# Optimization experiments

Measured on AMD Instinct MI355X. Metric: run time of the kernel, lower is better.

The kernel has to match this reference:

```python
import jax, jax.numpy as jnp
import numpy as np

H, KVH, HD, E, TOPK = 16, 4, 128, 8, 2
EPS = 1.1920929e-07  # fp32 machine eps, matches F.rms_norm default


def _rms(v):
    return v * jax.lax.rsqrt(jnp.mean(jnp.square(v), axis=-1, keepdims=True) + EPS)


def _rope(t, cos, sin):
    d = t.shape[-1] // 2
    t1, t2 = t[..., :d], t[..., d:]
    return jnp.concatenate([t1 * cos + t2 * sin, -t1 * sin + t2 * cos], axis=-1)


def setup_inputs():
    key = jax.random.key(0)
    ks = jax.random.split(key, 10)
    B, T, C, D = 2, 1024, 2048, 512
    # real rotary tables (broadcast over batch and heads)
    inv = 1.0 / (10000.0 ** (np.arange(HD // 2, dtype=np.float64) / (HD // 2)))
    ang = np.arange(T, dtype=np.float64)[:, None] * inv[None, :]
    cos = jnp.asarray(np.cos(ang), jnp.float32)[None, :, None, :]
    sin = jnp.asarray(np.sin(ang), jnp.float32)[None, :, None, :]
    w = lambda k, shp, fan: jax.random.normal(k, shp, jnp.float32) * (fan ** -0.5)
    return {
        'x': jax.random.normal(ks[0], (B, T, C), jnp.float32),
        'cos': cos, 'sin': sin,
        'Wq': w(ks[1], (C, C), C),
        'Wk': w(ks[2], (C, KVH * HD), C),
        'Wv': w(ks[3], (C, KVH * HD), C),
        'Wo': w(ks[4], (C, C), C),
        'Wr': w(ks[5], (C, E), C),
        'Ws1': w(ks[6], (C, D), C),
        'Ws2': w(ks[7], (D, C), D),
        'We1': w(ks[8], (E, C, D), C),
        'We2': w(ks[9], (E, D, C), D),
    }


def reference(x, cos, sin, Wq, Wk, Wv, Wo, Wr, Ws1, Ws2, We1, We2):
    B, T, C = x.shape
    # ---- attention (pre-norm, RoPE, QK-norm, GQA, causal SDPA) ----
    xn = _rms(x)
    q = _rms(_rope((xn @ Wq).reshape(B, T, H, HD), cos, sin))      # [B,T,H,HD]
    k = _rms(_rope((xn @ Wk).reshape(B, T, KVH, HD), cos, sin))    # [B,T,KVH,HD]
    v = (xn @ Wv).reshape(B, T, KVH, HD)
    rep = H // KVH
    k = jnp.repeat(k, rep, axis=2)
    v = jnp.repeat(v, rep, axis=2)
    scores = jnp.einsum('bthd,bshd->bhts', q, k) / np.float32(np.sqrt(HD))
    causal = jnp.tril(jnp.ones((T, T), bool))
    scores = jnp.where(causal, scores, jnp.float32(-np.inf))
    att = jax.nn.softmax(scores, axis=-1)
    y = jnp.einsum('bhts,bshd->bthd', att, v).reshape(B, T, C) @ Wo
    x = x + y
    # ---- DeepSeekMoE (shared expert + top-k routed experts) ----
    xf = _rms(x).reshape(-1, C)                                    # [N,C]
    N = xf.shape[0]
    shared = jnp.square(jax.nn.relu(xf @ Ws1)) @ Ws2               # [N,C]
    logits = xf @ Wr                                               # [N,E]
    tk_w, tk_idx = jax.lax.top_k(logits, TOPK)
    tk_w = jax.nn.softmax(tk_w.astype(jnp.float32), axis=-1).astype(x.dtype)
    # scatter top-k probs into dense per-expert gates (indices unique per row)
    gates = jnp.zeros((N, E), x.dtype).at[jnp.arange(N)[:, None], tk_idx].set(tk_w)
    h = jnp.square(jax.nn.relu(jnp.einsum('nc,ecd->end', xf, We1)))  # [E,N,D]
    routed = jnp.einsum('end,edc,ne->nc', h, We2, gates)             # [N,C]
    return x + (shared + routed).reshape(B, T, C)
```

## Files before the change

### kernel.cpp

```cpp
#include <hip/hip_runtime.h>

typedef _Float16 h16;
typedef _Float16 half8 __attribute__((ext_vector_type(8)));
typedef float f32x4 __attribute__((ext_vector_type(4)));

#define EPS_RMS 1.1920929e-07f
#define MiB (1ull << 20)

__device__ __forceinline__ void gload_lds16(const void* g, void* l) {
  __builtin_amdgcn_global_load_lds(
      (const __attribute__((address_space(1))) unsigned int*)g,
      (__attribute__((address_space(3))) unsigned int*)l, 16, 0, 0);
}

struct GemmP {
  const h16* Ah; const h16* Al;
  const h16* Bh; const h16* Bl;
  float* Cf; h16* Ch; h16* Cl;
  const float* R;
  const int* cnt; const int* off; const int* perm;
  long sAz, sBz, sCzHi, sCzLo;
  int M, N, K, lda, ldb, ldc;
  int zAoff, zBoff, zCoff, bzShift, czHiShift, czLoMask;
  float outScale;
};

template <int SPLIT, int EPI, int USECNT, int GATHER, int ASYNC>
__global__ __launch_bounds__(256, 4) void gemm_k(GemmP p) {
  constexpr int NP = SPLIT ? 2 : 1;
  constexpr int NBUF = (ASYNC == 1) ? 2 : 1;
  constexpr int APAD = (ASYNC == 1) ? 32 : 40;
  constexpr int BPAD = (ASYNC >= 1) ? 32 : 40;
  __shared__ __align__(16) h16 As[NBUF][NP][128][APAD];
  __shared__ __align__(16) h16 Bs[NBUF][NP][128][BPAD];
  __shared__ int permLds[GATHER ? 128 : 1];

  int bm, bn, zl;
  if constexpr (USECNT) {
    const int flat2d = blockIdx.y * gridDim.x + blockIdx.x;
    zl = flat2d & 7;
    const int idx = (flat2d >> 3) * 8 + blockIdx.z;
    bm = idx % gridDim.x;
    bn = idx / gridDim.x;
  } else {
    const int nwg = gridDim.x * gridDim.y;
    const int flat = blockIdx.y * gridDim.x + blockIdx.x;
    const int q8 = nwg >> 3, r8 = nwg & 7;
    const int xcd = flat & 7, sub = flat >> 3;
    const int swz = (xcd < r8 ? xcd * (q8 + 1) : r8 * (q8 + 1) + (xcd - r8) * q8) + sub;
    bm = swz % gridDim.x;
    bn = swz / gridDim.x;
    zl = blockIdx.z;
  }

  int Meff, rowbase;
  if (USECNT) {
    Meff = p.cnt[zl]; rowbase = p.off[zl];
    if (bm * 128 >= Meff) return;
  } else { Meff = p.M; rowbase = 0; }

  const int zA = zl + p.zAoff, zB = zl + p.zBoff, zC = zl + p.zCoff;
  const h16* Ah = p.Ah + (size_t)zA * p.sAz;
  const h16* Al = SPLIT ? p.Al + (size_t)zA * p.sAz : (const h16*)0;
  const size_t bofs = (size_t)(zB >> p.bzShift) * p.sBz;
  const h16* Bh = p.Bh + bofs;
  const h16* Bl = SPLIT ? p.Bl + bofs : (const h16*)0;
  const size_t cofs = (size_t)(zC >> p.czHiShift) * p.sCzHi +
                      (size_t)(zC & p.czLoMask) * p.sCzLo;

  const int tid = threadIdx.x;
  const int lane = tid & 63;
  const int wid = tid >> 6, wr = wid >> 1, wc = wid & 1;
  const int fr = lane & 15, fq = lane >> 4;

  if (GATHER) {
    if (tid < 128) {
      const int local = bm * 128 + tid;
      permLds[tid] = (local < Meff) ? p.perm[rowbase + local] : -1;
    }
    __syncthreads();
  }

  const long arow0 = (long)rowbase + (long)bm * 128;

  const f32x4 fz = {0.f, 0.f, 0.f, 0.f};
  f32x4 acc[4][4];
#pragma unroll
  for (int m = 0; m < 4; ++m)
#pragma unroll
    for (int n = 0; n < 4; ++n) acc[m][n] = fz;

  const int nkt = p.K / 32;

  auto compute = [&](int buf) {
    half8 af[NP][4], bf[NP][4];
#pragma unroll
    for (int m = 0; m < 4; ++m) {
      const int r = wr * 64 + m * 16 + fr;
      af[0][m] = *(const half8*)&As[buf][0][r][fq * 8];
      if (SPLIT) af[1][m] = *(const half8*)&As[buf][1][r][fq * 8];
    }
#pragma unroll
    for (int n = 0; n < 4; ++n) {
      const int c = wc * 64 + n * 16 + fr;
      bf[0][n] = *(const half8*)&Bs[buf][0][c][fq * 8];
      if (SPLIT) bf[1][n] = *(const half8*)&Bs[buf][1][c][fq * 8];
    }
#pragma unroll
    for (int m = 0; m < 4; ++m)
#pragma unroll
      for (int n = 0; n < 4; ++n) {
        acc[m][n] = __builtin_amdgcn_mfma_f32_16x16x32_f16(af[0][m], bf[0][n], acc[m][n], 0, 0, 0);
        if (SPLIT) {
          acc[m][n] = __builtin_amdgcn_mfma_f32_16x16x32_f16(af[0][m], bf[1][n], acc[m][n], 0, 0, 0);
          acc[m][n] = __builtin_amdgcn_mfma_f32_16x16x32_f16(af[1][m], bf[0][n], acc[m][n], 0, 0, 0);
        }
      }
  };

  if constexpr (ASYNC == 1) {
    auto stage = [&](int buf, int kt) {
      const int kb = kt * 32;
#pragma unroll
      for (int it = 0; it < 2; ++it) {
        const int d = (tid + it * 256) * 16;
        const int row = d >> 6;
        const int oct = (d >> 4) & 3;
        const size_t gb = ((size_t)(bn * 128 + row)) * p.ldb + kb + oct * 8;
        gload_lds16(Bh + gb, (char*)&Bs[buf][0][0][0] + d);
        if (SPLIT) gload_lds16(Bl + gb, (char*)&Bs[buf][1][0][0] + d);
        const size_t ga = (size_t)(arow0 + row) * p.lda + kb + oct * 8;
        gload_lds16(Ah + ga, (char*)&As[buf][0][0][0] + d);
        if (SPLIT) gload_lds16(Al + ga, (char*)&As[buf][1][0][0] + d);
      }
    };
    stage(0, 0);
    __syncthreads();
    int cur = 0;
    for (int kt = 0; kt < nkt; ++kt) {
      if (kt + 1 < nkt) stage(cur ^ 1, kt + 1);
      compute(cur);
      __syncthreads();
      cur ^= 1;
    }
  } else {
    for (int kt = 0; kt < nkt; ++kt) {
      if (kt) __syncthreads();
      const int kb = kt * 32;
      if constexpr (ASYNC == 2) {
#pragma unroll
        for (int it = 0; it < 2; ++it) {
          const int d = (tid + it * 256) * 16;
          const int row = d >> 6;
          const int oct = (d >> 4) & 3;
          const size_t gb = ((size_t)(bn * 128 + row)) * p.ldb + kb + oct * 8;
          gload_lds16(Bh + gb, (char*)&Bs[0][0][0][0] + d);
          if (SPLIT) gload_lds16(Bl + gb, (char*)&Bs[0][1][0][0] + d);
        }
      }
#pragma unroll
      for (int s = 0; s < 2; ++s) {
        const int seg = tid * 2 + s;
        const int row = seg >> 2, ks = (seg & 3) * 8;
        const int local = bm * 128 + row;
        bool av; long arow;
        if (GATHER) { const int tk2 = permLds[row]; av = (tk2 >= 0); arow = tk2; }
        else { av = (local < Meff); arow = (long)rowbase + local; }
        half8 vh = {0,0,0,0,0,0,0,0}, vl = {0,0,0,0,0,0,0,0};
        if (av) {
          vh = *(const half8*)(Ah + arow * (size_t)p.lda + kb + ks);
          if (SPLIT) vl = *(const half8*)(Al + arow * (size_t)p.lda + kb + ks);
        }
        *(half8*)&As[0][0][row][ks] = vh;
        if (SPLIT) *(half8*)&As[0][1][row][ks] = vl;
        if constexpr (ASYNC == 0) {
          const long brow = (long)bn * 128 + row;
          *(half8*)&Bs[0][0][row][ks] = *(const half8*)(Bh + brow * (size_t)p.ldb + kb + ks);
          if (SPLIT)
            *(half8*)&Bs[0][1][row][ks] = *(const half8*)(Bl + brow * (size_t)p.ldb + kb + ks);
        }
      }
      __syncthreads();
      compute(0);
    }
  }

#pragma unroll
  for (int m = 0; m < 4; ++m)
#pragma unroll
    for (int n = 0; n < 4; ++n)
#pragma unroll
      for (int j = 0; j < 4; ++j) {
        const int rl = wr * 64 + m * 16 + fq * 4 + j;
        const int cl = wc * 64 + n * 16 + fr;
        const int local = bm * 128 + rl;
        if (local >= Meff) continue;
        const size_t idx = cofs + ((size_t)rowbase + local) * p.ldc + (size_t)bn * 128 + cl;
        const float v = acc[m][n][j] * p.outScale;
        if (EPI == 0) p.Cf[idx] = v;
        else if (EPI == 1) p.Cf[idx] = v + p.R[idx];
        else if (EPI == 2) {
          const h16 hh = (h16)v;
          p.Ch[idx] = hh; p.Cl[idx] = (h16)(v - (float)hh);
        } else if (EPI == 3) {
          const float r2 = v > 0.f ? v * v : 0.f;
          p.Ch[idx] = (h16)r2;
        } else {
          p.Ch[idx] = (h16)v;
        }
      }
}

__global__ __launch_bounds__(512, 1) void flash_k(
    const h16* __restrict__ Qh, const h16* __restrict__ Ql,
    const h16* __restrict__ Kh, const h16* __restrict__ Kl,
    const h16* __restrict__ Vh, const h16* __restrict__ Vl,
    h16* __restrict__ yh, h16* __restrict__ yl) {
  __shared__ __align__(16) h16 Ks[2][32][136];
  __shared__ __align__(16) h16 Vs[2][128][40];
  __shared__ __align__(16) h16 Ps[8][2][16][40];

  const int qb = blockIdx.x, z = blockIdx.y;
  const int b = z >> 4, h = z & 15;
  const size_t qoff = (size_t)z * 131072;
  const size_t koff = (size_t)(b * 4 + (h >> 2)) * 131072;

  const int tid = threadIdx.x;
  const int lane = tid & 63, w = tid >> 6;
  const int fr = lane & 15, fq = lane >> 4;

  const int qrow = qb * 128 + w * 16 + fr;
  half8 qa[2][4];
#pragma unroll
  for (int kt = 0; kt < 4; ++kt) {
    qa[0][kt] = *(const half8*)(Qh + qoff + (size_t)qrow * 128 + kt * 32 + fq * 8);
    qa[1][kt] = *(const half8*)(Ql + qoff + (size_t)qrow * 128 + kt * 32 + fq * 8);
  }

  const int kRow = tid >> 4, kSeg = tid & 15;
  const int vRow = tid >> 2, vSeg = tid & 3;

  const f32x4 fz = {0.f, 0.f, 0.f, 0.f};
  f32x4 y[8];
#pragma unroll
  for (int n = 0; n < 8; ++n) y[n] = fz;
  float mrow[4] = {-3.0e38f, -3.0e38f, -3.0e38f, -3.0e38f};
  float lrow[4] = {0.f, 0.f, 0.f, 0.f};

  const int nt = (qb + 1) * 4;
  for (int t = 0; t < nt; ++t) {
    const int kvb = t * 32;
    if (t) __syncthreads();
#pragma unroll
    for (int pl = 0; pl < 2; ++pl) {
      const h16* kp = pl ? Kl : Kh;
      const h16* vp = pl ? Vl : Vh;
      *(half8*)&Ks[pl][kRow][kSeg * 8] =
          *(const half8*)(kp + koff + (size_t)(kvb + kRow) * 128 + kSeg * 8);
      *(half8*)&Vs[pl][vRow][vSeg * 8] =
          *(const half8*)(vp + koff + (size_t)vRow * 1024 + kvb + vSeg * 8);
    }
    __syncthreads();

    f32x4 sf[2] = {fz, fz};
#pragma unroll
    for (int n = 0; n < 2; ++n)
#pragma unroll
      for (int kt = 0; kt < 4; ++kt) {
        const half8 bh2 = *(const half8*)&Ks[0][n * 16 + fr][kt * 32 + fq * 8];
        const half8 bl2 = *(const half8*)&Ks[1][n * 16 + fr][kt * 32 + fq * 8];
        sf[n] = __builtin_amdgcn_mfma_f32_16x16x32_f16(qa[0][kt], bh2, sf[n], 0, 0, 0);
        sf[n] = __builtin_amdgcn_mfma_f32_16x16x32_f16(qa[0][kt], bl2, sf[n], 0, 0, 0);
        sf[n] = __builtin_amdgcn_mfma_f32_16x16x32_f16(qa[1][kt], bh2, sf[n], 0, 0, 0);
      }

    if (kvb + 31 > qb * 128) {
#pragma unroll
      for (int n = 0; n < 2; ++n)
#pragma unroll
        for (int j = 0; j < 4; ++j) {
          const int kvg = kvb + n * 16 + fr;
          const int qg = qb * 128 + w * 16 + fq * 4 + j;
          if (kvg > qg) sf[n][j] = -3.0e38f;
        }
    }

    float al[4];
#pragma unroll
    for (int j = 0; j < 4; ++j) {
      float tm = fmaxf(sf[0][j], sf[1][j]);
#pragma unroll
      for (int msk = 1; msk < 16; msk <<= 1) tm = fmaxf(tm, __shfl_xor(tm, msk, 16));
      const float mn = fmaxf(mrow[j], tm);
      al[j] = __expf(mrow[j] - mn);
      mrow[j] = mn;
      sf[0][j] = __expf(sf[0][j] - mn);
      sf[1][j] = __expf(sf[1][j] - mn);
      float ts = sf[0][j] + sf[1][j];
#pragma unroll
      for (int msk = 1; msk < 16; msk <<= 1) ts += __shfl_xor(ts, msk, 16);
      lrow[j] = lrow[j] * al[j] + ts;
    }
#pragma unroll
    for (int n = 0; n < 8; ++n)
#pragma unroll
      for (int j = 0; j < 4; ++j) y[n][j] *= al[j];

#pragma unroll
    for (int n = 0; n < 2; ++n)
#pragma unroll
      for (int j = 0; j < 4; ++j) {
        const float pp = sf[n][j] * 1024.f;
        const h16 hh = (h16)pp;
        Ps[w][0][fq * 4 + j][n * 16 + fr] = hh;
        Ps[w][1][fq * 4 + j][n * 16 + fr] = (h16)(pp - (float)hh);
      }

    const half8 pah = *(const half8*)&Ps[w][0][fr][fq * 8];
    const half8 pal = *(const half8*)&Ps[w][1][fr][fq * 8];
#pragma unroll
    for (int n = 0; n < 8; ++n) {
      const half8 vh2 = *(const half8*)&Vs[0][n * 16 + fr][fq * 8];
      const half8 vl2 = *(const half8*)&Vs[1][n * 16 + fr][fq * 8];
      y[n] = __builtin_amdgcn_mfma_f32_16x16x32_f16(pah, vh2, y[n], 0, 0, 0);
      y[n] = __builtin_amdgcn_mfma_f32_16x16x32_f16(pah, vl2, y[n], 0, 0, 0);
      y[n] = __builtin_amdgcn_mfma_f32_16x16x32_f16(pal, vh2, y[n], 0, 0, 0);
    }
  }

#pragma unroll
  for (int n = 0; n < 8; ++n)
#pragma unroll
    for (int j = 0; j < 4; ++j) {
      const int row = qb * 128 + w * 16 + fq * 4 + j;
      const int col = h * 128 + n * 16 + fr;
      const float v = y[n][j] / (1024.f * lrow[j]);
      const size_t idx = ((size_t)(b * 1024 + row)) * 2048 + col;
      const h16 hh = (h16)v;
      yh[idx] = hh; yl[idx] = (h16)(v - (float)hh);
    }
}

__global__ void tsplit_k(const float* __restrict__ W, h16* __restrict__ Th,
                         h16* __restrict__ Tl, int K, int N, float scale, int wantLo) {
  const size_t eoff = (size_t)blockIdx.z * (size_t)K * N;
  W += eoff; Th += eoff; if (Tl) Tl += eoff;
  __shared__ float tile[32][33];
  const int nt = blockIdx.x * 32, kt = blockIdx.y * 32;
  const int c = threadIdx.x & 31, r0 = threadIdx.x >> 5;
#pragma unroll
  for (int rr = 0; rr < 4; ++rr)
    tile[r0 + rr * 8][c] = W[(size_t)(kt + r0 + rr * 8) * N + nt + c];
  __syncthreads();
#pragma unroll
  for (int rr = 0; rr < 4; ++rr) {
    const int nrow = nt + r0 + rr * 8;
    const float v = tile[c][r0 + rr * 8] * scale;
    const h16 hh = (h16)v;
    Th[(size_t)nrow * K + kt + c] = hh;
    if (wantLo) Tl[(size_t)nrow * K + kt + c] = (h16)(v - (float)hh);
  }
}

template <int WLO, int WSC>
__global__ void rms_k(const float* __restrict__ X, h16* __restrict__ H,
                      h16* __restrict__ L, float* __restrict__ SC) {
  const int row = blockIdx.x;
  const float* x = X + (size_t)row * 2048;
  __shared__ float red[256];
  const int tid = threadIdx.x;
  float ss = 0.f;
  for (int c = tid; c < 2048; c += 256) { const float v = x[c]; ss += v * v; }
  red[tid] = ss; __syncthreads();
  for (int t = 128; t > 0; t >>= 1) {
    if (tid < t) red[tid] += red[tid + t];
    __syncthreads();
  }
  const float sc = rsqrtf(red[0] * (1.f / 2048.f) + EPS_RMS);
  if (WSC && tid == 0) SC[row] = sc;
  for (int c = tid; c < 2048; c += 256) {
    const float v = x[c] * sc;
    const size_t o2 = (size_t)row * 2048 + c;
    const h16 hh = (h16)v;
    H[o2] = hh;
    if (WLO) L[o2] = (h16)(v - (float)hh);
  }
}

__global__ void rope_k(const float* __restrict__ qkv, const float* __restrict__ cosT,
                       const float* __restrict__ sinT,
                       h16* __restrict__ Qh, h16* __restrict__ Ql,
                       h16* __restrict__ Kh, h16* __restrict__ Kl,
                       h16* __restrict__ Vh, h16* __restrict__ Vl) {
  const int tok = blockIdx.x;
  const int b = tok >> 10, t = tok & 1023;
  const int u = blockIdx.y, d = threadIdx.x;
  __shared__ float buf[128];
  __shared__ float red[128];
  int col;
  if (u < 16) col = u * 128 + d;
  else if (u < 20) col = 2048 + (u - 16) * 128 + d;
  else col = 2560 + (u - 20) * 128 + d;
  float v = qkv[(size_t)tok * 3072 + col];
  if (u < 20) {
    buf[d] = v; __syncthreads();
    float r;
    if (d < 64) {
      const float c = cosT[t * 64 + d], s = sinT[t * 64 + d];
      r = buf[d] * c + buf[d + 64] * s;
    } else {
      const float c = cosT[t * 64 + d - 64], s = sinT[t * 64 + d - 64];
      r = -buf[d - 64] * s + buf[d] * c;
    }
    red[d] = r * r; __syncthreads();
    for (int tt = 64; tt > 0; tt >>= 1) {
      if (d < tt) red[d] += red[d + tt];
      __syncthreads();
    }
    v = r * rsqrtf(red[0] * (1.f / 128.f) + EPS_RMS);
    if (u < 16) v *= 0.08838834764831845f;
  }
  const h16 hh = (h16)v;
  const h16 lo = (h16)(v - (float)hh);
  if (u < 16) {
    const size_t o2 = (((size_t)(b * 16 + u)) * 1024 + t) * 128 + d;
    Qh[o2] = hh; Ql[o2] = lo;
  } else if (u < 20) {
    const size_t o2 = (((size_t)(b * 4 + (u - 16))) * 1024 + t) * 128 + d;
    Kh[o2] = hh; Kl[o2] = lo;
  } else {
    const size_t o2 = ((size_t)(b * 4 + (u - 20))) * 131072 + (size_t)d * 1024 + t;
    Vh[o2] = hh; Vl[o2] = lo;
  }
}

__global__ void router_k(const float* __restrict__ x2, const float* __restrict__ rowscale,
                         const float* __restrict__ Wr,
                         int* __restrict__ idx2, float* __restrict__ g2,
                         int* __restrict__ cnt) {
  const int n = blockIdx.x;
  const int tid = threadIdx.x;
  __shared__ float red[256][8];
  float part[8] = {0, 0, 0, 0, 0, 0, 0, 0};
  for (int c = tid; c < 2048; c += 256) {
    const float v = x2[(size_t)n * 2048 + c];
    const float* w2 = Wr + (size_t)c * 8;
#pragma unroll
    for (int e = 0; e < 8; ++e) part[e] += v * w2[e];
  }
#pragma unroll
  for (int e = 0; e < 8; ++e) red[tid][e] = part[e];
  __syncthreads();
  for (int t = 128; t > 0; t >>= 1) {
    if (tid < t)
#pragma unroll
      for (int e = 0; e < 8; ++e) red[tid][e] += red[tid + t][e];
    __syncthreads();
  }
  if (tid == 0) {
    const float sc = rowscale[n];
    float l[8];
#pragma unroll
    for (int e = 0; e < 8; ++e) l[e] = red[0][e] * sc;
    int i1 = 0;
    for (int e = 1; e < 8; ++e) if (l[e] > l[i1]) i1 = e;
    int i2 = (i1 == 0) ? 1 : 0;
    for (int e = 0; e < 8; ++e) if (e != i1 && l[e] > l[i2]) i2 = e;
    const float e2 = __expf(l[i2] - l[i1]);
    const float inv = 1.f / (1.f + e2);
    idx2[n * 2] = i1; idx2[n * 2 + 1] = i2;
    g2[n * 2] = inv; g2[n * 2 + 1] = e2 * inv;
    atomicAdd(&cnt[i1], 1); atomicAdd(&cnt[i2], 1);
  }
}

__global__ void zero8_k(int* __restrict__ p) {
  if (threadIdx.x < 8 && blockIdx.x == 0) p[threadIdx.x] = 0;
}

__global__ void scan_k(const int* __restrict__ cnt, int* __restrict__ off,
                       int* __restrict__ base) {
  if (threadIdx.x == 0 && blockIdx.x == 0) {
    int a = 0;
    for (int e = 0; e < 8; ++e) { off[e] = a; base[e] = a; a += cnt[e]; }
  }
}

__global__ void assign_k(const int* __restrict__ idx2, int* __restrict__ base,
                         int* __restrict__ perm, int* __restrict__ pos2) {
  const int n = blockIdx.x * 256 + threadIdx.x;
  if (n >= 2048) return;
  for (int j = 0; j < 2; ++j) {
    const int e = idx2[n * 2 + j];
    const int pos = atomicAdd(&base[e], 1);
    perm[pos] = n;
    pos2[n * 2 + j] = pos;
  }
}

__global__ void combine_k(const float* __restrict__ x2, const h16* __restrict__ sh,
                          const h16* __restrict__ rp, const int* __restrict__ pos2,
                          const float* __restrict__ g2, float* __restrict__ out) {
  const int n = blockIdx.x;
  const int p0 = pos2[n * 2], p1 = pos2[n * 2 + 1];
  const float g0 = g2[n * 2], g1 = g2[n * 2 + 1];
  for (int c = threadIdx.x; c < 2048; c += 256) {
    const size_t i = (size_t)n * 2048 + c;
    out[i] = x2[i] + (float)sh[i] + g0 * (float)rp[(size_t)p0 * 2048 + c]
             + g1 * (float)rp[(size_t)p1 * 2048 + c];
  }
}

extern "C" void kernel_launch(void* const* d_in, const int* in_sizes, int n_in,
                              void* d_out, int out_size, void* d_ws, size_t ws_size,
                              hipStream_t stream) {
  const float* x    = (const float*)d_in[0];
  const float* cosT = (const float*)d_in[1];
  const float* sinT = (const float*)d_in[2];
  const float* Wq   = (const float*)d_in[3];
  const float* Wk   = (const float*)d_in[4];
  const float* Wv   = (const float*)d_in[5];
  const float* Wo   = (const float*)d_in[6];
  const float* Wr   = (const float*)d_in[7];
  const float* Ws1  = (const float*)d_in[8];
  const float* Ws2  = (const float*)d_in[9];
  const float* We1  = (const float*)d_in[10];
  const float* We2  = (const float*)d_in[11];
  float* out = (float*)d_out;

  unsigned char* W = (unsigned char*)d_ws;
  int*   idx2     = (int*)(W + 0);
  float* g2       = (float*)(W + 16 * 1024);
  int*   cnt      = (int*)(W + 32 * 1024);
  int*   offs     = (int*)(W + 33 * 1024);
  int*   base     = (int*)(W + 34 * 1024);
  int*   perm     = (int*)(W + 36 * 1024);
  int*   pos2     = (int*)(W + 52 * 1024);
  float* rowscale = (float*)(W + 68 * 1024);
  h16* W1h = (h16*)(W + 1 * MiB);
  h16* W1l = (h16*)(W + 13 * MiB);
  h16* W2h = (h16*)(W + 1 * MiB);
  h16* W2l = (h16*)(W + 9 * MiB);
  h16* xnh = (h16*)(W + 25 * MiB);
  h16* xnl = (h16*)(W + 33 * MiB);
  h16* yh  = (h16*)(W + 25 * MiB);
  h16* yl  = (h16*)(W + 33 * MiB);
  h16* xfh = (h16*)(W + 25 * MiB);
  h16* shh = (h16*)(W + 33 * MiB);
  float* qkv = (float*)(W + 41 * MiB);
  h16* hs    = (h16*)(W + 41 * MiB);
  h16* hperm = (h16*)(W + 43 * MiB);
  h16* Qh = (h16*)(W + 65 * MiB);
  h16* Ql = (h16*)(W + 73 * MiB);
  h16* Kh = (h16*)(W + 81 * MiB);
  h16* Kl = (h16*)(W + 83 * MiB);
  h16* Vh = (h16*)(W + 85 * MiB);
  h16* Vl = (h16*)(W + 87 * MiB);
  h16* rph = (h16*)(W + 65 * MiB);
  float* x2 = (float*)(W + 89 * MiB);
  h16* Ws1T = (h16*)(W + 105 * MiB);
  h16* Ws2T = (h16*)(W + 107 * MiB);
  h16* WeT  = (h16*)(W + 109 * MiB);

  const float WS = 64.f;
  const float IWS = 1.f / 64.f;

  tsplit_k<<<dim3(64, 64, 1), 256, 0, stream>>>(Wq, W1h, W1l, 2048, 2048, WS, 1);
  tsplit_k<<<dim3(16, 64, 1), 256, 0, stream>>>(Wk, W1h + (size_t)2048 * 2048,
                                                W1l + (size_t)2048 * 2048, 2048, 512, WS, 1);
  tsplit_k<<<dim3(16, 64, 1), 256, 0, stream>>>(Wv, W1h + (size_t)2560 * 2048,
                                                W1l + (size_t)2560 * 2048, 2048, 512, WS, 1);
  zero8_k<<<1, 64, 0, stream>>>(cnt);
  rms_k<1, 0><<<2048, 256, 0, stream>>>(x, xnh, xnl, (float*)0);
  {
    GemmP p{};
    p.Ah = xnh; p.Al = xnl; p.Bh = W1h; p.Bl = W1l; p.Cf = qkv;
    p.M = 2048; p.N = 3072; p.K = 2048; p.lda = 2048; p.ldb = 2048; p.ldc = 3072;
    p.outScale = IWS;
    gemm_k<1, 0, 0, 0, 1><<<dim3(16, 24, 1), 256, 0, stream>>>(p);
  }

  rope_k<<<dim3(2048, 24, 1), 128, 0, stream>>>(qkv, cosT, sinT, Qh, Ql, Kh, Kl, Vh, Vl);

  tsplit_k<<<dim3(64, 64, 1), 256, 0, stream>>>(Wo, W2h, W2l, 2048, 2048, WS, 1);
  flash_k<<<dim3(8, 32, 1), 512, 0, stream>>>(Qh, Ql, Kh, Kl, Vh, Vl, yh, yl);

  {
    GemmP p{};
    p.Ah = yh; p.Al = yl; p.Bh = W2h; p.Bl = W2l; p.Cf = x2; p.R = x;
    p.M = 2048; p.N = 2048; p.K = 2048; p.lda = 2048; p.ldb = 2048; p.ldc = 2048;
    p.outScale = IWS;
    gemm_k<1, 1, 0, 0, 1><<<dim3(16, 16, 1), 256, 0, stream>>>(p);
  }

  rms_k<0, 1><<<2048, 256, 0, stream>>>(x2, xfh, (h16*)0, rowscale);
  router_k<<<2048, 256, 0, stream>>>(x2, rowscale, Wr, idx2, g2, cnt);
  scan_k<<<1, 64, 0, stream>>>(cnt, offs, base);
  assign_k<<<8, 256, 0, stream>>>(idx2, base, perm, pos2);

  tsplit_k<<<dim3(16, 64, 1), 256, 0, stream>>>(Ws1, Ws1T, (h16*)0, 2048, 512, WS, 0);
  tsplit_k<<<dim3(64, 16, 1), 256, 0, stream>>>(Ws2, Ws2T, (h16*)0, 512, 2048, WS, 0);
  {
    GemmP p{};
    p.Ah = xfh; p.Bh = Ws1T; p.Ch = hs;
    p.M = 2048; p.N = 512; p.K = 2048; p.lda = 2048; p.ldb = 2048; p.ldc = 512;
    p.outScale = IWS;
    gemm_k<0, 3, 0, 0, 1><<<dim3(16, 4, 1), 256, 0, stream>>>(p);
  }
  {
    GemmP p{};
    p.Ah = hs; p.Bh = Ws2T; p.Ch = shh;
    p.M = 2048; p.N = 2048; p.K = 512; p.lda = 512; p.ldb = 512; p.ldc = 2048;
    p.outScale = IWS;
    gemm_k<0, 4, 0, 0, 1><<<dim3(16, 16, 1), 256, 0, stream>>>(p);
  }
  tsplit_k<<<dim3(16, 64, 8), 256, 0, stream>>>(We1, WeT, (h16*)0, 2048, 512, WS, 0);
  {
    GemmP p{};
    p.Ah = xfh; p.Bh = WeT; p.Ch = hperm;
    p.M = 2048; p.N = 512; p.K = 2048; p.lda = 2048; p.ldb = 2048; p.ldc = 512;
    p.sBz = (long)512 * 2048; p.bzShift = 0;
    p.cnt = cnt; p.off = offs; p.perm = perm;
    p.outScale = IWS;
    gemm_k<0, 3, 1, 1, 2><<<dim3(16, 4, 8), 256, 0, stream>>>(p);
  }
  tsplit_k<<<dim3(64, 16, 8), 256, 0, stream>>>(We2, WeT, (h16*)0, 512, 2048, WS, 0);
  {
    GemmP p{};
    p.Ah = hperm; p.Bh = WeT; p.Cf = (float*)0; p.Ch = rph;
    p.M = 2048; p.N = 2048; p.K = 512; p.lda = 512; p.ldb = 512; p.ldc = 2048;
    p.sBz = (long)2048 * 512; p.bzShift = 0;
    p.cnt = cnt; p.off = offs; p.perm = perm;
    p.outScale = IWS;
    gemm_k<0, 4, 1, 0, 1><<<dim3(16, 16, 8), 256, 0, stream>>>(p);
  }

  combine_k<<<2048, 256, 0, stream>>>(x2, shh, rph, pos2, g2, out);
}
```

Before: 585.2 us.

## Split long causal flash-attention query blocks across two KV chunks with combine kernel

Query blocks 4-7, which have the longest causal KV ranges, are now each split into two work items that process half of the KV tiles. Each half writes unnormalized partial outputs plus running max and sum to scratch, and a new combine kernel merges them with log-sum-exp rescaling. The aim is better load balance and more blocks to fill the GPU (384 instead of 256). The cost is extra fp32 scratch traffic and one more kernel launch.

```diff
diff --git a/kernel.cpp b/kernel.cpp
--- a/kernel.cpp
+++ b/kernel.cpp
@@ -215,12 +215,20 @@
     const h16* __restrict__ Qh, const h16* __restrict__ Ql,
     const h16* __restrict__ Kh, const h16* __restrict__ Kl,
     const h16* __restrict__ Vh, const h16* __restrict__ Vl,
-    h16* __restrict__ yh, h16* __restrict__ yl) {
+    h16* __restrict__ yh, h16* __restrict__ yl,
+    float* __restrict__ yp, float* __restrict__ mp, float* __restrict__ lp) {
   __shared__ __align__(16) h16 Ks[2][32][136];
   __shared__ __align__(16) h16 Vs[2][128][40];
   __shared__ __align__(16) h16 Ps[8][2][16][40];
 
-  const int qb = blockIdx.x, z = blockIdx.y;
+  const int item = blockIdx.x, z = blockIdx.y;
+  int qb, chunk;
+  if (item < 4) { qb = item; chunk = 0; }
+  else { qb = 4 + ((item - 4) >> 1); chunk = (item - 4) & 1; }
+  const int nt = (qb + 1) * 4;
+  const int tBeg = (item < 4) ? 0 : (chunk ? nt / 2 : 0);
+  const int tEnd = (item < 4) ? nt : (chunk ? nt : nt / 2);
+
   const int b = z >> 4, h = z & 15;
   const size_t qoff = (size_t)z * 131072;
   const size_t koff = (size_t)(b * 4 + (h >> 2)) * 131072;
@@ -247,10 +255,9 @@
   float mrow[4] = {-3.0e38f, -3.0e38f, -3.0e38f, -3.0e38f};
   float lrow[4] = {0.f, 0.f, 0.f, 0.f};
 
-  const int nt = (qb + 1) * 4;
-  for (int t = 0; t < nt; ++t) {
+  for (int t = tBeg; t < tEnd; ++t) {
     const int kvb = t * 32;
-    if (t) __syncthreads();
+    if (t != tBeg) __syncthreads();
 #pragma unroll
     for (int pl = 0; pl < 2; ++pl) {
       const h16* kp = pl ? Kl : Kh;
@@ -328,17 +335,53 @@
     }
   }
 
-#pragma unroll
-  for (int n = 0; n < 8; ++n)
+  if (item < 4) {
+#pragma unroll
+    for (int n = 0; n < 8; ++n)
+#pragma unroll
+      for (int j = 0; j < 4; ++j) {
+        const int row = qb * 128 + w * 16 + fq * 4 + j;
+        const int col = h * 128 + n * 16 + fr;
+        const float v = y[n][j] / (1024.f * lrow[j]);
+        const size_t idx = ((size_t)(b * 1024 + row)) * 2048 + col;
+        const h16 hh = (h16)v;
+        yh[idx] = hh; yl[idx] = (h16)(v - (float)hh);
+      }
+  } else {
 #pragma unroll
     for (int j = 0; j < 4; ++j) {
-      const int row = qb * 128 + w * 16 + fq * 4 + j;
-      const int col = h * 128 + n * 16 + fr;
-      const float v = y[n][j] / (1024.f * lrow[j]);
-      const size_t idx = ((size_t)(b * 1024 + row)) * 2048 + col;
-      const h16 hh = (h16)v;
-      yh[idx] = hh; yl[idx] = (h16)(v - (float)hh);
-    }
+      const int qrl = w * 16 + fq * 4 + j;
+      const int q512 = (qb - 4) * 128 + qrl;
+      const size_t rbase = (((size_t)chunk * 32 + z) * 512 + q512);
+#pragma unroll
+      for (int n = 0; n < 8; ++n)
+        yp[rbase * 128 + n * 16 + fr] = y[n][j];
+      if (fr == 0) { mp[rbase] = mrow[j]; lp[rbase] = lrow[j]; }
+    }
+  }
+}
+
+__global__ void comb_k(const float* __restrict__ yp, const float* __restrict__ mp,
+                       const float* __restrict__ lp,
+                       h16* __restrict__ yh, h16* __restrict__ yl) {
+  const int qh = blockIdx.x, z = blockIdx.y;
+  const int b = z >> 4, h = z & 15;
+  const int tid = threadIdx.x;
+  for (int idx = tid; idx < 16384; idx += 256) {
+    const int r = idx >> 7, d = idx & 127;
+    const int q512 = qh * 128 + r;
+    const size_t r0 = ((size_t)0 * 32 + z) * 512 + q512;
+    const size_t r1 = ((size_t)1 * 32 + z) * 512 + q512;
+    const float m1 = mp[r0], m2 = mp[r1];
+    const float l1 = lp[r0], l2 = lp[r1];
+    const float M = fmaxf(m1, m2);
+    const float e1 = __expf(m1 - M), e2 = __expf(m2 - M);
+    const float inv = 1.f / (1024.f * (l1 * e1 + l2 * e2));
+    const float v = (yp[r0 * 128 + d] * e1 + yp[r1 * 128 + d] * e2) * inv;
+    const size_t o = ((size_t)(b * 1024 + (4 + qh) * 128 + r)) * 2048 + h * 128 + d;
+    const h16 hh = (h16)v;
+    yh[o] = hh; yl[o] = (h16)(v - (float)hh);
+  }
 }
 
 __global__ void tsplit_k(const float* __restrict__ W, h16* __restrict__ Th,
@@ -548,6 +591,9 @@
   h16* xfh = (h16*)(W + 25 * MiB);
   h16* shh = (h16*)(W + 33 * MiB);
   float* qkv = (float*)(W + 41 * MiB);
+  float* ypart = (float*)(W + 41 * MiB);
+  float* mpart = (float*)(W + 57 * MiB);
+  float* lpart = (float*)(W + 58 * MiB);
   h16* hs    = (h16*)(W + 41 * MiB);
   h16* hperm = (h16*)(W + 43 * MiB);
   h16* Qh = (h16*)(W + 65 * MiB);
@@ -583,7 +629,9 @@
   rope_k<<<dim3(2048, 24, 1), 128, 0, stream>>>(qkv, cosT, sinT, Qh, Ql, Kh, Kl, Vh, Vl);
 
   tsplit_k<<<dim3(64, 64, 1), 256, 0, stream>>>(Wo, W2h, W2l, 2048, 2048, WS, 1);
-  flash_k<<<dim3(8, 32, 1), 512, 0, stream>>>(Qh, Ql, Kh, Kl, Vh, Vl, yh, yl);
+  flash_k<<<dim3(12, 32, 1), 512, 0, stream>>>(Qh, Ql, Kh, Kl, Vh, Vl, yh, yl,
+                                               ypart, mpart, lpart);
+  comb_k<<<dim3(4, 32, 1), 256, 0, stream>>>(ypart, mpart, lpart, yh, yl);
 
   {
     GemmP p{};
```

New measurement: 598.5 us. 2.3% more time.
